# Kernel optimization log

Hardware: AMD Instinct MI355X
Metric: run time of the kernel (lower is better)

## Reference

```python
import jax, jax.numpy as jnp
import numpy as np

B, N, DIN, DOUT, H, E = 8, 512, 128, 128, 8, 16
DH = DOUT // H
SCALE = float(np.sqrt(DH))


def _ln(x, g, b, eps=1e-5):
    m = jnp.mean(x, axis=-1, keepdims=True)
    v = jnp.mean((x - m) ** 2, axis=-1, keepdims=True)
    return (x - m) * jax.lax.rsqrt(v + eps) * g + b


def setup_inputs() -> dict:
    key = jax.random.key(0)
    ks = jax.random.split(key, 12)
    rn = lambda k, s: jax.random.normal(k, s, jnp.float32) * 0.05
    return {
        "x": jax.random.normal(ks[0], (B, N, DIN), jnp.float32),
        "adj": jax.random.randint(ks[1], (B, N, N), 0, 2, jnp.int32),
        "edge_attr": jax.random.normal(ks[2], (B, N, N, E), jnp.float32),
        "ln1_g": jnp.ones((DIN,), jnp.float32), "ln1_b": jnp.zeros((DIN,), jnp.float32),
        "Wp": rn(ks[3], (DIN, DOUT)), "bp": jnp.zeros((DOUT,), jnp.float32),
        "eln_g": jnp.ones((E,), jnp.float32), "eln_b": jnp.zeros((E,), jnp.float32),
        "We1": rn(ks[4], (E, 2 * E)), "be1": jnp.zeros((2 * E,), jnp.float32),
        "We2": rn(ks[5], (2 * E, H)), "be2": jnp.zeros((H,), jnp.float32),
        "Wq": rn(ks[6], (DOUT, DOUT)), "Wk": rn(ks[7], (DOUT, DOUT)), "Wv": rn(ks[8], (DOUT, DOUT)),
        "ffW1": rn(ks[9], (DOUT, 2 * DOUT)), "ffb1": jnp.zeros((2 * DOUT,), jnp.float32),
        "ffW2": rn(ks[10], (2 * DOUT, DOUT)), "ffb2": jnp.zeros((DOUT,), jnp.float32),
        "ln2_g": jnp.ones((DOUT,), jnp.float32), "ln2_b": jnp.zeros((DOUT,), jnp.float32),
    }


def reference(x, adj, edge_attr, ln1_g, ln1_b, Wp, bp, eln_g, eln_b, We1, be1, We2, be2,
              Wq, Wk, Wv, ffW1, ffb1, ffW2, ffb2, ln2_g, ln2_b):
    # Node projection after layer norm: [B,N,DOUT]
    xp = _ln(x, ln1_g, ln1_b) @ Wp + bp

    def heads(W):  # [B,H,N,DH]
        return (xp @ W).reshape(B, N, H, DH).transpose(0, 2, 1, 3)

    Q, K, V = heads(Wq), heads(Wk), heads(Wv)
    s = jnp.einsum('bhnd,bhmd->bhnm', Q, K) / SCALE  # [B,H,N,N]

    # Edge bias MLP: [B,N,N,E] -> [B,N,N,H] -> [B,H,N,N]
    eb = jax.nn.relu(_ln(edge_attr, eln_g, eln_b) @ We1 + be1) @ We2 + be2
    s = s + jnp.tanh(eb).transpose(0, 3, 1, 2) * 5.0

    # LeakyReLU(0.2)
    s = jnp.where(s >= 0, s, 0.2 * s)

    # adjacency mask with self-loops
    eye = jnp.eye(N, dtype=jnp.float32)[None]
    mask = jnp.minimum(adj.astype(jnp.float32) + eye, 1.0)[:, None]  # [B,1,N,N]
    neg_inf = jnp.finfo(s.dtype).min
    s = jnp.where(mask == 0, neg_inf, s)
    all_masked = jnp.all(mask == 0, axis=-1, keepdims=True)
    s = jnp.where(all_masked, 0.0, s)
    s = s - jnp.max(s, axis=-1, keepdims=True)
    p = jnp.nan_to_num(jax.nn.softmax(s, axis=-1))

    ctx = jnp.einsum('bhnm,bhmd->bhnd', p, V).transpose(0, 2, 1, 3).reshape(B, N, DOUT)
    h = xp + ctx
    ffn = jax.nn.relu(_ln(h, ln2_g, ln2_b) @ ffW1 + ffb1) @ ffW2 + ffb2
    return h + ffn
```

## Files before the change

kernel.cpp:

```cpp
#include <hip/hip_runtime.h>
#include <hip/hip_bf16.h>

#define BB 8
#define NN 512
#define DINC 128
#define DOUTC 128
#define HHC 8
#define EEC 16
#define DHC 16

typedef _Float16 h4 __attribute__((ext_vector_type(4)));
typedef float f32x4 __attribute__((ext_vector_type(4)));

__device__ __forceinline__ float wsum(float v){
#pragma unroll
  for (int o=1;o<64;o<<=1) v += __shfl_xor(v,o);
  return v;
}

__global__ __launch_bounds__(256) void k_proj(
    const float* __restrict__ x,
    const float* __restrict__ g1, const float* __restrict__ b1,
    const float* __restrict__ Wp, const float* __restrict__ bp,
    const float* __restrict__ Wq, const float* __restrict__ Wk, const float* __restrict__ Wv,
    float* __restrict__ xp, _Float16* __restrict__ Qh, _Float16* __restrict__ Kh, _Float16* __restrict__ Vh)
{
  __shared__ _Float16 xln[16][136];
  __shared__ _Float16 xps[16][136];
  __shared__ float    xp32[16][132];
  __shared__ _Float16 qs[3][16][136];
  int tid=threadIdx.x, w=tid>>6, lane=tid&63;
  int c=lane&15, g=lane>>4;
  int row0 = blockIdx.x*16;
  int b = row0>>9, n0 = row0&(NN-1);

  float ga=g1[lane], gb=g1[lane+64], ba=b1[lane], bbx=b1[lane+64];
#pragma unroll
  for (int rr=0;rr<4;++rr){
    int r = w + rr*4;
    size_t gi = (size_t)(row0+r)*DINC + lane;
    float a = x[gi], cc = x[gi+64];
    float s = wsum(a+cc);
    float q = wsum(a*a+cc*cc);
    float mean = s*(1.f/DINC);
    float var  = q*(1.f/DINC)-mean*mean;
    float rstd = rsqrtf(var+1e-5f);
    xln[r][lane]    = (_Float16)((a -mean)*rstd*ga + ba);
    xln[r][lane+64] = (_Float16)((cc-mean)*rstd*gb + bbx);
  }
  __syncthreads();

#pragma unroll
  for (int oo=0;oo<2;++oo){
    int ot = 2*w+oo;
    float4 bi = *(const float4*)(bp + 16*ot + 4*g);
    f32x4 D; D[0]=bi.x; D[1]=bi.y; D[2]=bi.z; D[3]=bi.w;
#pragma unroll
    for (int kt=0;kt<8;++kt){
      h4 f;
#pragma unroll
      for (int j=0;j<4;++j)
        f[j] = (_Float16)Wp[(size_t)(16*kt+4*g+j)*DOUTC + 16*ot + c];
      h4 hb = *(const h4*)&xln[c][16*kt+4*g];
      D = __builtin_amdgcn_mfma_f32_16x16x16f16(f, hb, D, 0,0,0);
    }
#pragma unroll
    for (int r=0;r<4;++r){
      xp32[c][16*ot+4*g+r] = D[r];
      xps [c][16*ot+4*g+r] = (_Float16)D[r];
    }
  }
  __syncthreads();

#pragma unroll
  for (int pp=0;pp<6;++pp){
    int p = w + pp*4;
    int mat = p>>3, ot = p&7;
    const float* W = (mat==0)? Wq : ((mat==1)? Wk : Wv);
    f32x4 D = {0.f,0.f,0.f,0.f};
#pragma unroll
    for (int kt=0;kt<8;++kt){
      h4 f;
#pragma unroll
      for (int j=0;j<4;++j)
        f[j] = (_Float16)W[(size_t)(16*kt+4*g+j)*DOUTC + 16*ot + c];
      h4 hb = *(const h4*)&xps[c][16*kt+4*g];
      D = __builtin_amdgcn_mfma_f32_16x16x16f16(f, hb, D, 0,0,0);
    }
#pragma unroll
    for (int r=0;r<4;++r)
      qs[mat][c][16*ot+4*g+r] = (_Float16)D[r];
  }
  __syncthreads();

#pragma unroll
  for (int i=tid;i<512;i+=256){
    int r=i>>5, seg=i&31;
    *(float4*)(xp + (size_t)(row0+r)*DOUTC + seg*4) = *(const float4*)&xp32[r][seg*4];
  }
#pragma unroll
  for (int mat=0;mat<3;++mat){
    int r = tid>>4, seg = tid&15;
    int h = seg>>1, d = (seg&1)*8;
    _Float16* O = (mat==0)? Qh : ((mat==1)? Kh : Vh);
    *(float4*)(O + (((size_t)b*HHC+h)*NN + n0+r)*DHC + d) = *(const float4*)&qs[mat][r][seg*8];
  }
}

__global__ __launch_bounds__(256) void k_edge(
  const float* __restrict__ ea, const int* __restrict__ adj,
  const float* __restrict__ eg, const float* __restrict__ ebi,
  const float* __restrict__ We1, const float* __restrict__ be1,
  const float* __restrict__ We2, const float* __restrict__ be2,
  _Float16* __restrict__ ebias)
{
  __shared__ _Float16 stage[8][520];
  __shared__ unsigned long long msk[8];
  __shared__ unsigned short idx16[512];
  __shared__ int cntS;

  int tid = threadIdx.x, w = tid>>6, lane = tid&63;
  int c = lane&15, g = lane>>4;
  int bn = blockIdx.x;
  int b = bn >> 9, n = bn & (NN-1);

  const int* adjRow = adj + (size_t)bn*NN;
  int col1 = tid, col2 = tid + 256;
  int v1 = (adjRow[col1] != 0) || (col1 == n);
  int v2 = (adjRow[col2] != 0) || (col2 == n);
  unsigned long long b1m = __ballot(v1);
  unsigned long long b2m = __ballot(v2);
  if (lane==0){ msk[w] = b1m; msk[4+w] = b2m; }

  h4 w1a,w1b,w2a,w2b;
#pragma unroll
  for (int j=0;j<4;++j){
    w1a[j] = (_Float16)We1[(4*g+j)*32 + c];
    w1b[j] = (_Float16)We1[(4*g+j)*32 + 16 + c];
    w2a[j] = (_Float16)((c<8)? We2[(4*g+j)*HHC + c] : 0.f);
    w2b[j] = (_Float16)((c<8)? We2[(16+4*g+j)*HHC + c] : 0.f);
  }
  float4 b1a = *(const float4*)(be1 + 4*g);
  float4 b1b = *(const float4*)(be1 + 16 + 4*g);
  float4 b2r = *(const float4*)(be2 + (g&1)*4);
  float4 G4  = *(const float4*)(eg  + 4*g);
  float4 Bv4 = *(const float4*)(ebi + 4*g);

  __syncthreads();

  int offs[8]; int cnt = 0;
#pragma unroll
  for (int k=0;k<8;++k){ offs[k] = cnt; cnt += __popcll(msk[k]); }
  if (tid==0) cntS = cnt;

  {
    _Float16 neg = (_Float16)(-30000.f);
    h4 negv; negv[0]=neg; negv[1]=neg; negv[2]=neg; negv[3]=neg;
#pragma unroll
    for (int i=tid;i<1024;i+=256){
      int h = i>>7, m4 = i&127;
      *(h4*)&stage[h][m4*4] = negv;
    }
  }

  if (v1){
    int pos = offs[w]   + __popcll(msk[w]   & ((1ull<<lane)-1ull));
    idx16[pos] = (unsigned short)col1;
  }
  if (v2){
    int pos = offs[4+w] + __popcll(msk[4+w] & ((1ull<<lane)-1ull));
    idx16[pos] = (unsigned short)col2;
  }
  __syncthreads();

  cnt = cntS;
  int nt = (cnt + 15) >> 4;
  const float* eaRow = ea + (size_t)bn*NN*EEC;

  for (int t = w; t < nt; t += 4){
    int slot = 16*t + c;
    int sidx = slot < cnt ? slot : cnt-1;
    int idx  = idx16[sidx];
    float4 v = *(const float4*)(eaRow + (size_t)idx*EEC + 4*g);
    float s = v.x+v.y+v.z+v.w;
    float q = v.x*v.x+v.y*v.y+v.z*v.z+v.w*v.w;
    s += __shfl_xor(s,16); s += __shfl_xor(s,32);
    q += __shfl_xor(q,16); q += __shfl_xor(q,32);
    float mean = s*(1.f/EEC);
    float var  = q*(1.f/EEC) - mean*mean;
    float rstd = rsqrtf(var + 1e-5f);
    h4 ef;
    ef[0]=(_Float16)((v.x-mean)*rstd*G4.x + Bv4.x);
    ef[1]=(_Float16)((v.y-mean)*rstd*G4.y + Bv4.y);
    ef[2]=(_Float16)((v.z-mean)*rstd*G4.z + Bv4.z);
    ef[3]=(_Float16)((v.w-mean)*rstd*G4.w + Bv4.w);
    f32x4 d1a = {b1a.x,b1a.y,b1a.z,b1a.w};
    f32x4 d1b = {b1b.x,b1b.y,b1b.z,b1b.w};
    d1a = __builtin_amdgcn_mfma_f32_16x16x16f16(w1a, ef, d1a, 0,0,0);
    d1b = __builtin_amdgcn_mfma_f32_16x16x16f16(w1b, ef, d1b, 0,0,0);
    h4 hfa,hfb;
#pragma unroll
    for (int r=0;r<4;++r){
      hfa[r]=(_Float16)fmaxf(d1a[r],0.f);
      hfb[r]=(_Float16)fmaxf(d1b[r],0.f);
    }
    f32x4 d2 = {0.f,0.f,0.f,0.f};
    d2 = __builtin_amdgcn_mfma_f32_16x16x16f16(w2a, hfa, d2, 0,0,0);
    d2 = __builtin_amdgcn_mfma_f32_16x16x16f16(w2b, hfb, d2, 0,0,0);
    if (g<2 && slot<cnt){
#pragma unroll
      for (int r=0;r<4;++r){
        float y = d2[r] + ((const float*)&b2r)[r];
        y = fminf(fmaxf(2.f*y,-30.f),30.f);
        float ex = __expf(y);
        float t2 = (ex-1.f)/(ex+1.f);
        stage[4*g+r][idx] = (_Float16)(5.f*t2);
      }
    }
  }
  __syncthreads();

  size_t base = ((size_t)b*HHC)*NN*NN + (size_t)n*NN;
#pragma unroll
  for (int i=tid;i<512;i+=256){
    int h = i>>6, m8 = i&63;
    *(float4*)(ebias + base + (size_t)h*NN*NN + m8*8) =
        *(const float4*)&stage[h][m8*8];
  }
}

__global__ __launch_bounds__(256) void k_attn(
  const _Float16* __restrict__ Qh, const _Float16* __restrict__ Kh, const _Float16* __restrict__ Vh,
  const _Float16* __restrict__ eb, float* __restrict__ ctxb)
{
  __shared__ _Float16 Klds[NN*DHC];
  __shared__ _Float16 Vt[DHC*520];
  int tid = threadIdx.x;
  int bh   = blockIdx.x >> 3;
  int tile = blockIdx.x & 7;
  const _Float16* Kg = Kh + (size_t)bh*NN*DHC;
  const _Float16* Vg = Vh + (size_t)bh*NN*DHC;
  {
    const float4* src = (const float4*)Kg;
    float4* dst = (float4*)Klds;
#pragma unroll
    for (int i=tid;i<1024;i+=256) dst[i]=src[i];
  }
  {
#pragma unroll
    for (int i=tid;i<1024;i+=256){
      int m = i>>1, hf = i&1;
      float4 v4 = *(const float4*)(Vg + (size_t)m*DHC + hf*8);
      const _Float16* hh = (const _Float16*)&v4;
#pragma unroll
      for (int jj=0;jj<8;++jj) Vt[(hf*8+jj)*520 + m] = hh[jj];
    }
  }
  __syncthreads();

  int w = tid>>6, lane = tid&63;
  int c = lane&15, g = lane>>4;
  int n0 = tile*64 + w*16;

  h4 qf = *(const h4*)(Qh + ((size_t)bh*NN + n0 + c)*DHC + 4*g);
  const _Float16* ebw = eb + ((size_t)bh*NN + n0 + c)*NN + 4*g;

  f32x4 zero = {0.f,0.f,0.f,0.f};
  f32x4 acc = zero;
  float rowsum = 0.f;
#pragma unroll
  for (int t=0;t<32;++t){
    h4 kf = *(const h4*)(Klds + (16*t + c)*DHC + 4*g);
    f32x4 d = __builtin_amdgcn_mfma_f32_16x16x16f16(kf, qf, zero, 0, 0, 0);
    h4 e4 = *(const h4*)(ebw + 16*t);
    h4 pa;
#pragma unroll
    for (int r=0;r<4;++r){
      float sv = d[r]*0.25f + (float)e4[r];
      sv = fmaxf(sv,0.f) + 0.2f*fminf(sv,0.f);
      float p = __expf(sv - 6.f);
      rowsum += p;
      pa[r] = (_Float16)p;
    }
    h4 vf = *(const h4*)(Vt + c*520 + 16*t + 4*g);
    acc = __builtin_amdgcn_mfma_f32_16x16x16f16(pa, vf, acc, 0, 0, 0);
  }
  rowsum += __shfl_xor(rowsum,16);
  rowsum += __shfl_xor(rowsum,32);

  int b = bh>>3, h = bh&7;
#pragma unroll
  for (int r=0;r<4;++r){
    float sr = __shfl(rowsum, g*16 + 4*g + r);
    ctxb[((size_t)b*NN + n0 + 4*g + r)*DOUTC + h*DHC + c] = acc[r]/sr;
  }
}

__global__ __launch_bounds__(256) void k_ffn(
  const float* __restrict__ xp, const float* __restrict__ ctxb,
  const float* __restrict__ g2, const float* __restrict__ b2v,
  const float* __restrict__ W1, const float* __restrict__ bb1,
  const float* __restrict__ W2, const float* __restrict__ bb2,
  float* __restrict__ out)
{
  __shared__ float    hrow[8][DOUTC];
  __shared__ _Float16 hn[16][136];
  __shared__ float    part[4][8][16][16];

  int tid = threadIdx.x, w = tid>>6, lane = tid&63;
  int c = lane&15, g = lane>>4;
  int n0 = blockIdx.x * 8;

#pragma unroll
  for (int i=tid;i<272;i+=256){
    h4 z = {(_Float16)0.f,(_Float16)0.f,(_Float16)0.f,(_Float16)0.f};
    ((h4*)hn)[272+i] = z;
  }

  float ga=g2[lane], gb=g2[lane+64], ba=b2v[lane], bbx=b2v[lane+64];
#pragma unroll
  for (int rr=0;rr<2;++rr){
    int r = w + rr*4;
    size_t gi = (size_t)(n0+r)*DOUTC + lane;
    float a  = xp[gi]    + ctxb[gi];
    float cc = xp[gi+64] + ctxb[gi+64];
    hrow[r][lane] = a; hrow[r][lane+64] = cc;
    float s = wsum(a+cc);
    float q = wsum(a*a+cc*cc);
    float mean = s*(1.f/DOUTC);
    float var  = q*(1.f/DOUTC) - mean*mean;
    float rstd = rsqrtf(var + 1e-5f);
    hn[r][lane]    = (_Float16)((a -mean)*rstd*ga + ba);
    hn[r][lane+64] = (_Float16)((cc-mean)*rstd*gb + bbx);
  }
  __syncthreads();

  h4 hidB[4];
#pragma unroll
  for (int t=0;t<4;++t){
    int ht = 4*w + t;
    float4 bi = *(const float4*)(bb1 + 16*ht + 4*g);
    f32x4 D1; D1[0]=bi.x; D1[1]=bi.y; D1[2]=bi.z; D1[3]=bi.w;
#pragma unroll
    for (int kt=0;kt<8;++kt){
      h4 f;
#pragma unroll
      for (int j=0;j<4;++j)
        f[j] = (_Float16)W1[(size_t)(16*kt + 4*g + j)*256 + 16*ht + c];
      h4 hb = *(const h4*)&hn[c][16*kt + 4*g];
      D1 = __builtin_amdgcn_mfma_f32_16x16x16f16(f, hb, D1, 0,0,0);
    }
#pragma unroll
    for (int r=0;r<4;++r) hidB[t][r] = (_Float16)fmaxf(D1[r], 0.f);
  }

#pragma unroll
  for (int ot=0;ot<8;++ot){
    f32x4 d2 = {0.f,0.f,0.f,0.f};
#pragma unroll
    for (int t=0;t<4;++t){
      h4 f;
#pragma unroll
      for (int j=0;j<4;++j)
        f[j] = (_Float16)W2[(size_t)(16*(4*w+t) + 4*g + j)*128 + 16*ot + c];
      d2 = __builtin_amdgcn_mfma_f32_16x16x16f16(f, hidB[t], d2, 0,0,0);
    }
#pragma unroll
    for (int r=0;r<4;++r) part[w][ot][4*g+r][c] = d2[r];
  }
  __syncthreads();

#pragma unroll
  for (int i=tid;i<1024;i+=256){
    int n = i>>7, col = i&127;
    int ot = col>>4, m = col&15;
    float v = part[0][ot][m][n] + part[1][ot][m][n]
            + part[2][ot][m][n] + part[3][ot][m][n];
    out[(size_t)(n0+n)*DOUTC + col] = hrow[n][col] + v + bb2[col];
  }
}

extern "C" void kernel_launch(void* const* d_in, const int* in_sizes, int n_in,
                              void* d_out, int out_size, void* d_ws, size_t ws_size,
                              hipStream_t stream)
{
  const float* x     = (const float*)d_in[0];
  const int*   adj   = (const int*)  d_in[1];
  const float* ea    = (const float*)d_in[2];
  const float* ln1_g = (const float*)d_in[3];
  const float* ln1_b = (const float*)d_in[4];
  const float* Wp    = (const float*)d_in[5];
  const float* bp    = (const float*)d_in[6];
  const float* eln_g = (const float*)d_in[7];
  const float* eln_b = (const float*)d_in[8];
  const float* We1   = (const float*)d_in[9];
  const float* be1   = (const float*)d_in[10];
  const float* We2   = (const float*)d_in[11];
  const float* be2   = (const float*)d_in[12];
  const float* Wq    = (const float*)d_in[13];
  const float* Wk    = (const float*)d_in[14];
  const float* Wv    = (const float*)d_in[15];
  const float* ffW1  = (const float*)d_in[16];
  const float* ffb1  = (const float*)d_in[17];
  const float* ffW2  = (const float*)d_in[18];
  const float* ffb2  = (const float*)d_in[19];
  const float* ln2_g = (const float*)d_in[20];
  const float* ln2_b = (const float*)d_in[21];
  float* out = (float*)d_out;

  char* ws = (char*)d_ws;
  float*    xp  = (float*)(ws);
  float*    ctx = (float*)(ws + ((size_t)2<<20));
  _Float16* Qh  = (_Float16*)(ws + ((size_t)4<<20));
  _Float16* Kh  = (_Float16*)(ws + ((size_t)5<<20));
  _Float16* Vh  = (_Float16*)(ws + ((size_t)6<<20));
  _Float16* ebf = (_Float16*)(ws + ((size_t)7<<20));

  k_proj<<<(BB*NN)/16, 256, 0, stream>>>(x, ln1_g, ln1_b, Wp, bp, Wq, Wk, Wv, xp, Qh, Kh, Vh);
  k_edge<<<BB*NN, 256, 0, stream>>>(ea, adj, eln_g, eln_b, We1, be1, We2, be2, ebf);
  k_attn<<<BB*HHC*8, 256, 0, stream>>>(Qh, Kh, Vh, ebf, ctx);
  k_ffn<<<(BB*NN)/8, 256, 0, stream>>>(xp, ctx, ln2_g, ln2_b, ffW1, ffb1, ffW2, ffb2, out);
}
```

Before: 79.88 us.

## Merge projection and edge kernels into one launch, restructure edge LN per lane

Combines k_proj and k_edge into a single kernel whose blocks dispatch on blockIdx to either projection or edge work, sharing one shared-memory buffer. This removes one launch and lets the two independent stages run concurrently. The edge path now gives each lane a whole 16-wide edge row for layer norm and stages the results through LDS for four MFMA tiles per wave. xp is stored in fp16 instead of fp32 to cut write and read traffic, at some cost in accuracy for the residual.

```diff
diff --git a/kernel.cpp b/kernel.cpp
--- a/kernel.cpp
+++ b/kernel.cpp
@@ -8,6 +8,7 @@
 #define HHC 8
 #define EEC 16
 #define DHC 16
+#define NPROJ 256
 
 typedef _Float16 h4 __attribute__((ext_vector_type(4)));
 typedef float f32x4 __attribute__((ext_vector_type(4)));
@@ -18,20 +19,21 @@
   return v;
 }
 
-__global__ __launch_bounds__(256) void k_proj(
+
+__device__ __forceinline__ void proj_body(
+    char* smem, int blk,
     const float* __restrict__ x,
     const float* __restrict__ g1, const float* __restrict__ b1,
     const float* __restrict__ Wp, const float* __restrict__ bp,
     const float* __restrict__ Wq, const float* __restrict__ Wk, const float* __restrict__ Wv,
-    float* __restrict__ xp, _Float16* __restrict__ Qh, _Float16* __restrict__ Kh, _Float16* __restrict__ Vh)
-{
-  __shared__ _Float16 xln[16][136];
-  __shared__ _Float16 xps[16][136];
-  __shared__ float    xp32[16][132];
-  __shared__ _Float16 qs[3][16][136];
+    _Float16* __restrict__ xph, _Float16* __restrict__ Qh, _Float16* __restrict__ Kh, _Float16* __restrict__ Vh)
+{
+  _Float16 (*xln)[136] = (_Float16(*)[136])(smem);
+  _Float16 (*xps)[136] = (_Float16(*)[136])(smem + 4352);
+  _Float16* qs         = (_Float16*)(smem + 8704);
   int tid=threadIdx.x, w=tid>>6, lane=tid&63;
   int c=lane&15, g=lane>>4;
-  int row0 = blockIdx.x*16;
+  int row0 = blk*16;
   int b = row0>>9, n0 = row0&(NN-1);
 
   float ga=g1[lane], gb=g1[lane+64], ba=b1[lane], bbx=b1[lane+64];
@@ -65,10 +67,8 @@
       D = __builtin_amdgcn_mfma_f32_16x16x16f16(f, hb, D, 0,0,0);
     }
 #pragma unroll
-    for (int r=0;r<4;++r){
-      xp32[c][16*ot+4*g+r] = D[r];
-      xps [c][16*ot+4*g+r] = (_Float16)D[r];
-    }
+    for (int r=0;r<4;++r)
+      xps[c][16*ot+4*g+r] = (_Float16)D[r];
   }
   __syncthreads();
 
@@ -89,39 +89,39 @@
     }
 #pragma unroll
     for (int r=0;r<4;++r)
-      qs[mat][c][16*ot+4*g+r] = (_Float16)D[r];
-  }
-  __syncthreads();
-
-#pragma unroll
-  for (int i=tid;i<512;i+=256){
-    int r=i>>5, seg=i&31;
-    *(float4*)(xp + (size_t)(row0+r)*DOUTC + seg*4) = *(const float4*)&xp32[r][seg*4];
+      qs[(mat*16 + c)*136 + 16*ot+4*g+r] = (_Float16)D[r];
+  }
+  __syncthreads();
+
+  {
+    int r = tid>>4, seg = tid&15;
+    *(float4*)(xph + (size_t)(row0+r)*DOUTC + seg*8) = *(const float4*)&xps[r][seg*8];
   }
 #pragma unroll
   for (int mat=0;mat<3;++mat){
     int r = tid>>4, seg = tid&15;
     int h = seg>>1, d = (seg&1)*8;
     _Float16* O = (mat==0)? Qh : ((mat==1)? Kh : Vh);
-    *(float4*)(O + (((size_t)b*HHC+h)*NN + n0+r)*DHC + d) = *(const float4*)&qs[mat][r][seg*8];
-  }
-}
-
-__global__ __launch_bounds__(256) void k_edge(
-  const float* __restrict__ ea, const int* __restrict__ adj,
-  const float* __restrict__ eg, const float* __restrict__ ebi,
-  const float* __restrict__ We1, const float* __restrict__ be1,
-  const float* __restrict__ We2, const float* __restrict__ be2,
-  _Float16* __restrict__ ebias)
-{
-  __shared__ _Float16 stage[8][520];
-  __shared__ unsigned long long msk[8];
-  __shared__ unsigned short idx16[512];
-  __shared__ int cntS;
+    *(float4*)(O + (((size_t)b*HHC+h)*NN + n0+r)*DHC + d) = *(const float4*)&qs[(mat*16+r)*136 + seg*8];
+  }
+}
+
+__device__ __forceinline__ void edge_body(
+    char* smem, int bn,
+    const float* __restrict__ ea, const int* __restrict__ adj,
+    const float* __restrict__ eg, const float* __restrict__ ebi,
+    const float* __restrict__ We1, const float* __restrict__ be1,
+    const float* __restrict__ We2, const float* __restrict__ be2,
+    _Float16* __restrict__ ebias)
+{
+  _Float16* ef              = (_Float16*)(smem);
+  _Float16 (*stage)[520]    = (_Float16(*)[520])(smem + 12288);
+  unsigned short* idx16     = (unsigned short*)(smem + 20608);
+  unsigned long long* msk   = (unsigned long long*)(smem + 21632);
+  int* cntS                 = (int*)(smem + 21696);
 
   int tid = threadIdx.x, w = tid>>6, lane = tid&63;
   int c = lane&15, g = lane>>4;
-  int bn = blockIdx.x;
   int b = bn >> 9, n = bn & (NN-1);
 
   const int* adjRow = adj + (size_t)bn*NN;
@@ -140,18 +140,16 @@
     w2a[j] = (_Float16)((c<8)? We2[(4*g+j)*HHC + c] : 0.f);
     w2b[j] = (_Float16)((c<8)? We2[(16+4*g+j)*HHC + c] : 0.f);
   }
+  float4 b2r = *(const float4*)(be2 + (g&1)*4);
   float4 b1a = *(const float4*)(be1 + 4*g);
   float4 b1b = *(const float4*)(be1 + 16 + 4*g);
-  float4 b2r = *(const float4*)(be2 + (g&1)*4);
-  float4 G4  = *(const float4*)(eg  + 4*g);
-  float4 Bv4 = *(const float4*)(ebi + 4*g);
 
   __syncthreads();
 
   int offs[8]; int cnt = 0;
 #pragma unroll
   for (int k=0;k<8;++k){ offs[k] = cnt; cnt += __popcll(msk[k]); }
-  if (tid==0) cntS = cnt;
+  if (tid==0) *cntS = cnt;
 
   {
     _Float16 neg = (_Float16)(-30000.f);
@@ -173,48 +171,59 @@
   }
   __syncthreads();
 
-  cnt = cntS;
-  int nt = (cnt + 15) >> 4;
+  cnt = *cntS;
+  int ng = (cnt + 63) >> 6;
   const float* eaRow = ea + (size_t)bn*NN*EEC;
 
-  for (int t = w; t < nt; t += 4){
-    int slot = 16*t + c;
+  for (int grp = w; grp < ng; grp += 4){
+    int slot = grp*64 + lane;
     int sidx = slot < cnt ? slot : cnt-1;
     int idx  = idx16[sidx];
-    float4 v = *(const float4*)(eaRow + (size_t)idx*EEC + 4*g);
-    float s = v.x+v.y+v.z+v.w;
-    float q = v.x*v.x+v.y*v.y+v.z*v.z+v.w*v.w;
-    s += __shfl_xor(s,16); s += __shfl_xor(s,32);
-    q += __shfl_xor(q,16); q += __shfl_xor(q,32);
+    const float4* ep = (const float4*)(eaRow + (size_t)idx*EEC);
+    float4 a0=ep[0], a1=ep[1], a2=ep[2], a3=ep[3];
+    float e[16] = {a0.x,a0.y,a0.z,a0.w, a1.x,a1.y,a1.z,a1.w,
+                   a2.x,a2.y,a2.z,a2.w, a3.x,a3.y,a3.z,a3.w};
+    float s=0.f, q=0.f;
+#pragma unroll
+    for (int k=0;k<16;++k){ s+=e[k]; q+=e[k]*e[k]; }
     float mean = s*(1.f/EEC);
     float var  = q*(1.f/EEC) - mean*mean;
     float rstd = rsqrtf(var + 1e-5f);
-    h4 ef;
-    ef[0]=(_Float16)((v.x-mean)*rstd*G4.x + Bv4.x);
-    ef[1]=(_Float16)((v.y-mean)*rstd*G4.y + Bv4.y);
-    ef[2]=(_Float16)((v.z-mean)*rstd*G4.z + Bv4.z);
-    ef[3]=(_Float16)((v.w-mean)*rstd*G4.w + Bv4.w);
-    f32x4 d1a = {b1a.x,b1a.y,b1a.z,b1a.w};
-    f32x4 d1b = {b1b.x,b1b.y,b1b.z,b1b.w};
-    d1a = __builtin_amdgcn_mfma_f32_16x16x16f16(w1a, ef, d1a, 0,0,0);
-    d1b = __builtin_amdgcn_mfma_f32_16x16x16f16(w1b, ef, d1b, 0,0,0);
-    h4 hfa,hfb;
-#pragma unroll
-    for (int r=0;r<4;++r){
-      hfa[r]=(_Float16)fmaxf(d1a[r],0.f);
-      hfb[r]=(_Float16)fmaxf(d1b[r],0.f);
-    }
-    f32x4 d2 = {0.f,0.f,0.f,0.f};
-    d2 = __builtin_amdgcn_mfma_f32_16x16x16f16(w2a, hfa, d2, 0,0,0);
-    d2 = __builtin_amdgcn_mfma_f32_16x16x16f16(w2b, hfb, d2, 0,0,0);
-    if (g<2 && slot<cnt){
+    _Float16 ef16[16];
+#pragma unroll
+    for (int k=0;k<16;++k)
+      ef16[k] = (_Float16)((e[k]-mean)*rstd*eg[k] + ebi[k]);
+    _Float16* dst = ef + (size_t)(w*64 + lane)*24;
+    *(float4*)(dst)     = *(const float4*)&ef16[0];
+    *(float4*)(dst + 8) = *(const float4*)&ef16[8];
+
+#pragma unroll
+    for (int tt=0;tt<4;++tt){
+      h4 efr = *(const h4*)(ef + (size_t)(w*64 + tt*16 + c)*24 + 4*g);
+      f32x4 d1a = {b1a.x,b1a.y,b1a.z,b1a.w};
+      f32x4 d1b = {b1b.x,b1b.y,b1b.z,b1b.w};
+      d1a = __builtin_amdgcn_mfma_f32_16x16x16f16(w1a, efr, d1a, 0,0,0);
+      d1b = __builtin_amdgcn_mfma_f32_16x16x16f16(w1b, efr, d1b, 0,0,0);
+      h4 hfa,hfb;
 #pragma unroll
       for (int r=0;r<4;++r){
-        float y = d2[r] + ((const float*)&b2r)[r];
-        y = fminf(fmaxf(2.f*y,-30.f),30.f);
-        float ex = __expf(y);
-        float t2 = (ex-1.f)/(ex+1.f);
-        stage[4*g+r][idx] = (_Float16)(5.f*t2);
+        hfa[r]=(_Float16)fmaxf(d1a[r],0.f);
+        hfb[r]=(_Float16)fmaxf(d1b[r],0.f);
+      }
+      f32x4 d2 = {0.f,0.f,0.f,0.f};
+      d2 = __builtin_amdgcn_mfma_f32_16x16x16f16(w2a, hfa, d2, 0,0,0);
+      d2 = __builtin_amdgcn_mfma_f32_16x16x16f16(w2b, hfb, d2, 0,0,0);
+      int slot2 = grp*64 + tt*16 + c;
+      if (g<2 && slot2<cnt){
+        int sidx2 = idx16[slot2];
+#pragma unroll
+        for (int r=0;r<4;++r){
+          float y = d2[r] + ((const float*)&b2r)[r];
+          y = fminf(fmaxf(2.f*y,-30.f),30.f);
+          float ex = __expf(y);
+          float t2 = (ex-1.f)/(ex+1.f);
+          stage[4*g+r][sidx2] = (_Float16)(5.f*t2);
+        }
       }
     }
   }
@@ -227,6 +236,26 @@
     *(float4*)(ebias + base + (size_t)h*NN*NN + m8*8) =
         *(const float4*)&stage[h][m8*8];
   }
+}
+
+__global__ __launch_bounds__(256) void k_projedge(
+    const float* __restrict__ x,
+    const float* __restrict__ g1, const float* __restrict__ b1,
+    const float* __restrict__ Wp, const float* __restrict__ bp,
+    const float* __restrict__ Wq, const float* __restrict__ Wk, const float* __restrict__ Wv,
+    _Float16* __restrict__ xph, _Float16* __restrict__ Qh, _Float16* __restrict__ Kh, _Float16* __restrict__ Vh,
+    const float* __restrict__ ea, const int* __restrict__ adj,
+    const float* __restrict__ eg, const float* __restrict__ ebi,
+    const float* __restrict__ We1, const float* __restrict__ be1,
+    const float* __restrict__ We2, const float* __restrict__ be2,
+    _Float16* __restrict__ ebias)
+{
+  __shared__ __align__(16) char smem[21760];
+  int blk = blockIdx.x;
+  if (blk < NPROJ)
+    proj_body(smem, blk, x, g1, b1, Wp, bp, Wq, Wk, Wv, xph, Qh, Kh, Vh);
+  else
+    edge_body(smem, blk - NPROJ, ea, adj, eg, ebi, We1, be1, We2, be2, ebias);
 }
 
 __global__ __launch_bounds__(256) void k_attn(
@@ -297,7 +326,7 @@
 }
 
 __global__ __launch_bounds__(256) void k_ffn(
-  const float* __restrict__ xp, const float* __restrict__ ctxb,
+  const _Float16* __restrict__ xph, const float* __restrict__ ctxb,
   const float* __restrict__ g2, const float* __restrict__ b2v,
   const float* __restrict__ W1, const float* __restrict__ bb1,
   const float* __restrict__ W2, const float* __restrict__ bb2,
@@ -322,8 +351,8 @@
   for (int rr=0;rr<2;++rr){
     int r = w + rr*4;
     size_t gi = (size_t)(n0+r)*DOUTC + lane;
-    float a  = xp[gi]    + ctxb[gi];
-    float cc = xp[gi+64] + ctxb[gi+64];
+    float a  = (float)xph[gi]    + ctxb[gi];
+    float cc = (float)xph[gi+64] + ctxb[gi+64];
     hrow[r][lane] = a; hrow[r][lane+64] = cc;
     float s = wsum(a+cc);
     float q = wsum(a*a+cc*cc);
@@ -409,15 +438,16 @@
   float* out = (float*)d_out;
 
   char* ws = (char*)d_ws;
-  float*    xp  = (float*)(ws);
+  _Float16* xph = (_Float16*)(ws);
   float*    ctx = (float*)(ws + ((size_t)2<<20));
   _Float16* Qh  = (_Float16*)(ws + ((size_t)4<<20));
   _Float16* Kh  = (_Float16*)(ws + ((size_t)5<<20));
   _Float16* Vh  = (_Float16*)(ws + ((size_t)6<<20));
   _Float16* ebf = (_Float16*)(ws + ((size_t)7<<20));
 
-  k_proj<<<(BB*NN)/16, 256, 0, stream>>>(x, ln1_g, ln1_b, Wp, bp, Wq, Wk, Wv, xp, Qh, Kh, Vh);
-  k_edge<<<BB*NN, 256, 0, stream>>>(ea, adj, eln_g, eln_b, We1, be1, We2, be2, ebf);
+  k_projedge<<<NPROJ + BB*NN, 256, 0, stream>>>(
+      x, ln1_g, ln1_b, Wp, bp, Wq, Wk, Wv, xph, Qh, Kh, Vh,
+      ea, adj, eln_g, eln_b, We1, be1, We2, be2, ebf);
   k_attn<<<BB*HHC*8, 256, 0, stream>>>(Qh, Kh, Vh, ebf, ctx);
-  k_ffn<<<(BB*NN)/8, 256, 0, stream>>>(xp, ctx, ln2_g, ln2_b, ffW1, ffb1, ffW2, ffb2, out);
-}
+  k_ffn<<<(BB*NN)/8, 256, 0, stream>>>(xph, ctx, ln2_g, ln2_b, ffW1, ffb1, ffW2, ffb2, out);
+}
```

After: 89.23 us. +11.7%, slower.

## Merge projection and edge-bias kernels into one launch; store xp in fp16

Applied to the files above, without the earlier changes.

Combines the node projection kernel and the edge-bias MLP kernel into a single grid. Edge blocks come first and projection blocks are appended, which removes one launch and lets the two independent stages overlap on the GPU. The residual xp is also stored as fp16 instead of fp32, so k_ffn reads half as many bytes for it. The cost is lower precision in the residual path, and every block now reserves the combined shared memory of both stages, which may reduce occupancy.

```diff
diff --git a/kernel.cpp b/kernel.cpp
--- a/kernel.cpp
+++ b/kernel.cpp
@@ -8,6 +8,7 @@
 #define HHC 8
 #define EEC 16
 #define DHC 16
+#define NEDGE (BB*NN)
 
 typedef _Float16 h4 __attribute__((ext_vector_type(4)));
 typedef float f32x4 __attribute__((ext_vector_type(4)));
@@ -18,214 +19,209 @@
   return v;
 }
 
-__global__ __launch_bounds__(256) void k_proj(
+__global__ __launch_bounds__(256) void k_projedge(
     const float* __restrict__ x,
     const float* __restrict__ g1, const float* __restrict__ b1,
     const float* __restrict__ Wp, const float* __restrict__ bp,
     const float* __restrict__ Wq, const float* __restrict__ Wk, const float* __restrict__ Wv,
-    float* __restrict__ xp, _Float16* __restrict__ Qh, _Float16* __restrict__ Kh, _Float16* __restrict__ Vh)
-{
-  __shared__ _Float16 xln[16][136];
-  __shared__ _Float16 xps[16][136];
-  __shared__ float    xp32[16][132];
-  __shared__ _Float16 qs[3][16][136];
-  int tid=threadIdx.x, w=tid>>6, lane=tid&63;
-  int c=lane&15, g=lane>>4;
-  int row0 = blockIdx.x*16;
-  int b = row0>>9, n0 = row0&(NN-1);
-
-  float ga=g1[lane], gb=g1[lane+64], ba=b1[lane], bbx=b1[lane+64];
-#pragma unroll
-  for (int rr=0;rr<4;++rr){
-    int r = w + rr*4;
-    size_t gi = (size_t)(row0+r)*DINC + lane;
-    float a = x[gi], cc = x[gi+64];
-    float s = wsum(a+cc);
-    float q = wsum(a*a+cc*cc);
-    float mean = s*(1.f/DINC);
-    float var  = q*(1.f/DINC)-mean*mean;
-    float rstd = rsqrtf(var+1e-5f);
-    xln[r][lane]    = (_Float16)((a -mean)*rstd*ga + ba);
-    xln[r][lane+64] = (_Float16)((cc-mean)*rstd*gb + bbx);
-  }
-  __syncthreads();
-
-#pragma unroll
-  for (int oo=0;oo<2;++oo){
-    int ot = 2*w+oo;
-    float4 bi = *(const float4*)(bp + 16*ot + 4*g);
-    f32x4 D; D[0]=bi.x; D[1]=bi.y; D[2]=bi.z; D[3]=bi.w;
-#pragma unroll
-    for (int kt=0;kt<8;++kt){
-      h4 f;
-#pragma unroll
-      for (int j=0;j<4;++j)
-        f[j] = (_Float16)Wp[(size_t)(16*kt+4*g+j)*DOUTC + 16*ot + c];
-      h4 hb = *(const h4*)&xln[c][16*kt+4*g];
-      D = __builtin_amdgcn_mfma_f32_16x16x16f16(f, hb, D, 0,0,0);
-    }
-#pragma unroll
-    for (int r=0;r<4;++r){
-      xp32[c][16*ot+4*g+r] = D[r];
-      xps [c][16*ot+4*g+r] = (_Float16)D[r];
-    }
-  }
-  __syncthreads();
-
-#pragma unroll
-  for (int pp=0;pp<6;++pp){
-    int p = w + pp*4;
-    int mat = p>>3, ot = p&7;
-    const float* W = (mat==0)? Wq : ((mat==1)? Wk : Wv);
-    f32x4 D = {0.f,0.f,0.f,0.f};
-#pragma unroll
-    for (int kt=0;kt<8;++kt){
-      h4 f;
-#pragma unroll
-      for (int j=0;j<4;++j)
-        f[j] = (_Float16)W[(size_t)(16*kt+4*g+j)*DOUTC + 16*ot + c];
-      h4 hb = *(const h4*)&xps[c][16*kt+4*g];
-      D = __builtin_amdgcn_mfma_f32_16x16x16f16(f, hb, D, 0,0,0);
-    }
-#pragma unroll
-    for (int r=0;r<4;++r)
-      qs[mat][c][16*ot+4*g+r] = (_Float16)D[r];
-  }
-  __syncthreads();
-
-#pragma unroll
-  for (int i=tid;i<512;i+=256){
-    int r=i>>5, seg=i&31;
-    *(float4*)(xp + (size_t)(row0+r)*DOUTC + seg*4) = *(const float4*)&xp32[r][seg*4];
-  }
-#pragma unroll
-  for (int mat=0;mat<3;++mat){
-    int r = tid>>4, seg = tid&15;
-    int h = seg>>1, d = (seg&1)*8;
-    _Float16* O = (mat==0)? Qh : ((mat==1)? Kh : Vh);
-    *(float4*)(O + (((size_t)b*HHC+h)*NN + n0+r)*DHC + d) = *(const float4*)&qs[mat][r][seg*8];
-  }
-}
-
-__global__ __launch_bounds__(256) void k_edge(
-  const float* __restrict__ ea, const int* __restrict__ adj,
-  const float* __restrict__ eg, const float* __restrict__ ebi,
-  const float* __restrict__ We1, const float* __restrict__ be1,
-  const float* __restrict__ We2, const float* __restrict__ be2,
-  _Float16* __restrict__ ebias)
+    _Float16* __restrict__ xph, _Float16* __restrict__ Qh, _Float16* __restrict__ Kh, _Float16* __restrict__ Vh,
+    const float* __restrict__ ea, const int* __restrict__ adj,
+    const float* __restrict__ eg, const float* __restrict__ ebi,
+    const float* __restrict__ We1, const float* __restrict__ be1,
+    const float* __restrict__ We2, const float* __restrict__ be2,
+    _Float16* __restrict__ ebias)
 {
   __shared__ _Float16 stage[8][520];
   __shared__ unsigned long long msk[8];
   __shared__ unsigned short idx16[512];
   __shared__ int cntS;
+  __shared__ _Float16 xln[16][136];
+  __shared__ _Float16 xps[16][136];
+  __shared__ _Float16 qs[3][16][136];
 
   int tid = threadIdx.x, w = tid>>6, lane = tid&63;
   int c = lane&15, g = lane>>4;
-  int bn = blockIdx.x;
-  int b = bn >> 9, n = bn & (NN-1);
-
-  const int* adjRow = adj + (size_t)bn*NN;
-  int col1 = tid, col2 = tid + 256;
-  int v1 = (adjRow[col1] != 0) || (col1 == n);
-  int v2 = (adjRow[col2] != 0) || (col2 == n);
-  unsigned long long b1m = __ballot(v1);
-  unsigned long long b2m = __ballot(v2);
-  if (lane==0){ msk[w] = b1m; msk[4+w] = b2m; }
-
-  h4 w1a,w1b,w2a,w2b;
-#pragma unroll
-  for (int j=0;j<4;++j){
-    w1a[j] = (_Float16)We1[(4*g+j)*32 + c];
-    w1b[j] = (_Float16)We1[(4*g+j)*32 + 16 + c];
-    w2a[j] = (_Float16)((c<8)? We2[(4*g+j)*HHC + c] : 0.f);
-    w2b[j] = (_Float16)((c<8)? We2[(16+4*g+j)*HHC + c] : 0.f);
-  }
-  float4 b1a = *(const float4*)(be1 + 4*g);
-  float4 b1b = *(const float4*)(be1 + 16 + 4*g);
-  float4 b2r = *(const float4*)(be2 + (g&1)*4);
-  float4 G4  = *(const float4*)(eg  + 4*g);
-  float4 Bv4 = *(const float4*)(ebi + 4*g);
-
-  __syncthreads();
-
-  int offs[8]; int cnt = 0;
-#pragma unroll
-  for (int k=0;k<8;++k){ offs[k] = cnt; cnt += __popcll(msk[k]); }
-  if (tid==0) cntS = cnt;
-
-  {
-    _Float16 neg = (_Float16)(-30000.f);
-    h4 negv; negv[0]=neg; negv[1]=neg; negv[2]=neg; negv[3]=neg;
-#pragma unroll
-    for (int i=tid;i<1024;i+=256){
-      int h = i>>7, m4 = i&127;
-      *(h4*)&stage[h][m4*4] = negv;
-    }
-  }
-
-  if (v1){
-    int pos = offs[w]   + __popcll(msk[w]   & ((1ull<<lane)-1ull));
-    idx16[pos] = (unsigned short)col1;
-  }
-  if (v2){
-    int pos = offs[4+w] + __popcll(msk[4+w] & ((1ull<<lane)-1ull));
-    idx16[pos] = (unsigned short)col2;
-  }
-  __syncthreads();
-
-  cnt = cntS;
-  int nt = (cnt + 15) >> 4;
-  const float* eaRow = ea + (size_t)bn*NN*EEC;
-
-  for (int t = w; t < nt; t += 4){
-    int slot = 16*t + c;
-    int sidx = slot < cnt ? slot : cnt-1;
-    int idx  = idx16[sidx];
-    float4 v = *(const float4*)(eaRow + (size_t)idx*EEC + 4*g);
-    float s = v.x+v.y+v.z+v.w;
-    float q = v.x*v.x+v.y*v.y+v.z*v.z+v.w*v.w;
-    s += __shfl_xor(s,16); s += __shfl_xor(s,32);
-    q += __shfl_xor(q,16); q += __shfl_xor(q,32);
-    float mean = s*(1.f/EEC);
-    float var  = q*(1.f/EEC) - mean*mean;
-    float rstd = rsqrtf(var + 1e-5f);
-    h4 ef;
-    ef[0]=(_Float16)((v.x-mean)*rstd*G4.x + Bv4.x);
-    ef[1]=(_Float16)((v.y-mean)*rstd*G4.y + Bv4.y);
-    ef[2]=(_Float16)((v.z-mean)*rstd*G4.z + Bv4.z);
-    ef[3]=(_Float16)((v.w-mean)*rstd*G4.w + Bv4.w);
-    f32x4 d1a = {b1a.x,b1a.y,b1a.z,b1a.w};
-    f32x4 d1b = {b1b.x,b1b.y,b1b.z,b1b.w};
-    d1a = __builtin_amdgcn_mfma_f32_16x16x16f16(w1a, ef, d1a, 0,0,0);
-    d1b = __builtin_amdgcn_mfma_f32_16x16x16f16(w1b, ef, d1b, 0,0,0);
-    h4 hfa,hfb;
-#pragma unroll
-    for (int r=0;r<4;++r){
-      hfa[r]=(_Float16)fmaxf(d1a[r],0.f);
-      hfb[r]=(_Float16)fmaxf(d1b[r],0.f);
-    }
-    f32x4 d2 = {0.f,0.f,0.f,0.f};
-    d2 = __builtin_amdgcn_mfma_f32_16x16x16f16(w2a, hfa, d2, 0,0,0);
-    d2 = __builtin_amdgcn_mfma_f32_16x16x16f16(w2b, hfb, d2, 0,0,0);
-    if (g<2 && slot<cnt){
+
+  if (blockIdx.x < NEDGE){
+    int bn = blockIdx.x;
+    int b = bn >> 9, n = bn & (NN-1);
+
+    const int* adjRow = adj + (size_t)bn*NN;
+    int col1 = tid, col2 = tid + 256;
+    int v1 = (adjRow[col1] != 0) || (col1 == n);
+    int v2 = (adjRow[col2] != 0) || (col2 == n);
+    unsigned long long b1m = __ballot(v1);
+    unsigned long long b2m = __ballot(v2);
+    if (lane==0){ msk[w] = b1m; msk[4+w] = b2m; }
+
+    h4 w1a,w1b,w2a,w2b;
+#pragma unroll
+    for (int j=0;j<4;++j){
+      w1a[j] = (_Float16)We1[(4*g+j)*32 + c];
+      w1b[j] = (_Float16)We1[(4*g+j)*32 + 16 + c];
+      w2a[j] = (_Float16)((c<8)? We2[(4*g+j)*HHC + c] : 0.f);
+      w2b[j] = (_Float16)((c<8)? We2[(16+4*g+j)*HHC + c] : 0.f);
+    }
+    float4 b1a = *(const float4*)(be1 + 4*g);
+    float4 b1b = *(const float4*)(be1 + 16 + 4*g);
+    float4 b2r = *(const float4*)(be2 + (g&1)*4);
+    float4 G4  = *(const float4*)(eg  + 4*g);
+    float4 Bv4 = *(const float4*)(ebi + 4*g);
+
+    __syncthreads();
+
+    int offs[8]; int cnt = 0;
+#pragma unroll
+    for (int k=0;k<8;++k){ offs[k] = cnt; cnt += __popcll(msk[k]); }
+    if (tid==0) cntS = cnt;
+
+    {
+      _Float16 neg = (_Float16)(-30000.f);
+      h4 negv; negv[0]=neg; negv[1]=neg; negv[2]=neg; negv[3]=neg;
+#pragma unroll
+      for (int i=tid;i<1024;i+=256){
+        int h = i>>7, m4 = i&127;
+        *(h4*)&stage[h][m4*4] = negv;
+      }
+    }
+
+    if (v1){
+      int pos = offs[w]   + __popcll(msk[w]   & ((1ull<<lane)-1ull));
+      idx16[pos] = (unsigned short)col1;
+    }
+    if (v2){
+      int pos = offs[4+w] + __popcll(msk[4+w] & ((1ull<<lane)-1ull));
+      idx16[pos] = (unsigned short)col2;
+    }
+    __syncthreads();
+
+    cnt = cntS;
+    int nt = (cnt + 15) >> 4;
+    const float* eaRow = ea + (size_t)bn*NN*EEC;
+
+    for (int t = w; t < nt; t += 4){
+      int slot = 16*t + c;
+      int sidx = slot < cnt ? slot : cnt-1;
+      int idx  = idx16[sidx];
+      float4 v = *(const float4*)(eaRow + (size_t)idx*EEC + 4*g);
+      float s = v.x+v.y+v.z+v.w;
+      float q = v.x*v.x+v.y*v.y+v.z*v.z+v.w*v.w;
+      s += __shfl_xor(s,16); s += __shfl_xor(s,32);
+      q += __shfl_xor(q,16); q += __shfl_xor(q,32);
+      float mean = s*(1.f/EEC);
+      float var  = q*(1.f/EEC) - mean*mean;
+      float rstd = rsqrtf(var + 1e-5f);
+      h4 ef;
+      ef[0]=(_Float16)((v.x-mean)*rstd*G4.x + Bv4.x);
+      ef[1]=(_Float16)((v.y-mean)*rstd*G4.y + Bv4.y);
+      ef[2]=(_Float16)((v.z-mean)*rstd*G4.z + Bv4.z);
+      ef[3]=(_Float16)((v.w-mean)*rstd*G4.w + Bv4.w);
+      f32x4 d1a = {b1a.x,b1a.y,b1a.z,b1a.w};
+      f32x4 d1b = {b1b.x,b1b.y,b1b.z,b1b.w};
+      d1a = __builtin_amdgcn_mfma_f32_16x16x16f16(w1a, ef, d1a, 0,0,0);
+      d1b = __builtin_amdgcn_mfma_f32_16x16x16f16(w1b, ef, d1b, 0,0,0);
+      h4 hfa,hfb;
 #pragma unroll
       for (int r=0;r<4;++r){
-        float y = d2[r] + ((const float*)&b2r)[r];
-        y = fminf(fmaxf(2.f*y,-30.f),30.f);
-        float ex = __expf(y);
-        float t2 = (ex-1.f)/(ex+1.f);
-        stage[4*g+r][idx] = (_Float16)(5.f*t2);
+        hfa[r]=(_Float16)fmaxf(d1a[r],0.f);
+        hfb[r]=(_Float16)fmaxf(d1b[r],0.f);
       }
-    }
-  }
-  __syncthreads();
-
-  size_t base = ((size_t)b*HHC)*NN*NN + (size_t)n*NN;
-#pragma unroll
-  for (int i=tid;i<512;i+=256){
-    int h = i>>6, m8 = i&63;
-    *(float4*)(ebias + base + (size_t)h*NN*NN + m8*8) =
-        *(const float4*)&stage[h][m8*8];
+      f32x4 d2 = {0.f,0.f,0.f,0.f};
+      d2 = __builtin_amdgcn_mfma_f32_16x16x16f16(w2a, hfa, d2, 0,0,0);
+      d2 = __builtin_amdgcn_mfma_f32_16x16x16f16(w2b, hfb, d2, 0,0,0);
+      if (g<2 && slot<cnt){
+#pragma unroll
+        for (int r=0;r<4;++r){
+          float y = d2[r] + ((const float*)&b2r)[r];
+          y = fminf(fmaxf(2.f*y,-30.f),30.f);
+          float ex = __expf(y);
+          float t2 = (ex-1.f)/(ex+1.f);
+          stage[4*g+r][idx] = (_Float16)(5.f*t2);
+        }
+      }
+    }
+    __syncthreads();
+
+    size_t base = ((size_t)b*HHC)*NN*NN + (size_t)n*NN;
+#pragma unroll
+    for (int i=tid;i<512;i+=256){
+      int h = i>>6, m8 = i&63;
+      *(float4*)(ebias + base + (size_t)h*NN*NN + m8*8) =
+          *(const float4*)&stage[h][m8*8];
+    }
+  } else {
+    int blk = blockIdx.x - NEDGE;
+    int row0 = blk*16;
+    int b = row0>>9, n0 = row0&(NN-1);
+
+    float ga=g1[lane], gb=g1[lane+64], ba=b1[lane], bbx=b1[lane+64];
+#pragma unroll
+    for (int rr=0;rr<4;++rr){
+      int r = w + rr*4;
+      size_t gi = (size_t)(row0+r)*DINC + lane;
+      float a = x[gi], cc = x[gi+64];
+      float s = wsum(a+cc);
+      float q = wsum(a*a+cc*cc);
+      float mean = s*(1.f/DINC);
+      float var  = q*(1.f/DINC)-mean*mean;
+      float rstd = rsqrtf(var+1e-5f);
+      xln[r][lane]    = (_Float16)((a -mean)*rstd*ga + ba);
+      xln[r][lane+64] = (_Float16)((cc-mean)*rstd*gb + bbx);
+    }
+    __syncthreads();
+
+#pragma unroll
+    for (int oo=0;oo<2;++oo){
+      int ot = 2*w+oo;
+      float4 bi = *(const float4*)(bp + 16*ot + 4*g);
+      f32x4 D; D[0]=bi.x; D[1]=bi.y; D[2]=bi.z; D[3]=bi.w;
+#pragma unroll
+      for (int kt=0;kt<8;++kt){
+        h4 f;
+#pragma unroll
+        for (int j=0;j<4;++j)
+          f[j] = (_Float16)Wp[(size_t)(16*kt+4*g+j)*DOUTC + 16*ot + c];
+        h4 hb = *(const h4*)&xln[c][16*kt+4*g];
+        D = __builtin_amdgcn_mfma_f32_16x16x16f16(f, hb, D, 0,0,0);
+      }
+#pragma unroll
+      for (int r=0;r<4;++r)
+        xps[c][16*ot+4*g+r] = (_Float16)D[r];
+    }
+    __syncthreads();
+
+#pragma unroll
+    for (int pp=0;pp<6;++pp){
+      int p = w + pp*4;
+      int mat = p>>3, ot = p&7;
+      const float* W = (mat==0)? Wq : ((mat==1)? Wk : Wv);
+      f32x4 D = {0.f,0.f,0.f,0.f};
+#pragma unroll
+      for (int kt=0;kt<8;++kt){
+        h4 f;
+#pragma unroll
+        for (int j=0;j<4;++j)
+          f[j] = (_Float16)W[(size_t)(16*kt+4*g+j)*DOUTC + 16*ot + c];
+        h4 hb = *(const h4*)&xps[c][16*kt+4*g];
+        D = __builtin_amdgcn_mfma_f32_16x16x16f16(f, hb, D, 0,0,0);
+      }
+#pragma unroll
+      for (int r=0;r<4;++r)
+        qs[mat][c][16*ot+4*g+r] = (_Float16)D[r];
+    }
+    __syncthreads();
+
+    {
+      int r = tid>>4, seg = tid&15;
+      *(float4*)(xph + (size_t)(row0+r)*DOUTC + seg*8) = *(const float4*)&xps[r][seg*8];
+    }
+#pragma unroll
+    for (int mat=0;mat<3;++mat){
+      int r = tid>>4, seg = tid&15;
+      int h = seg>>1, d = (seg&1)*8;
+      _Float16* O = (mat==0)? Qh : ((mat==1)? Kh : Vh);
+      *(float4*)(O + (((size_t)b*HHC+h)*NN + n0+r)*DHC + d) = *(const float4*)&qs[mat][r][seg*8];
+    }
   }
 }
 
@@ -297,7 +293,7 @@
 }
 
 __global__ __launch_bounds__(256) void k_ffn(
-  const float* __restrict__ xp, const float* __restrict__ ctxb,
+  const _Float16* __restrict__ xph, const float* __restrict__ ctxb,
   const float* __restrict__ g2, const float* __restrict__ b2v,
   const float* __restrict__ W1, const float* __restrict__ bb1,
   const float* __restrict__ W2, const float* __restrict__ bb2,
@@ -322,8 +318,8 @@
   for (int rr=0;rr<2;++rr){
     int r = w + rr*4;
     size_t gi = (size_t)(n0+r)*DOUTC + lane;
-    float a  = xp[gi]    + ctxb[gi];
-    float cc = xp[gi+64] + ctxb[gi+64];
+    float a  = (float)xph[gi]    + ctxb[gi];
+    float cc = (float)xph[gi+64] + ctxb[gi+64];
     hrow[r][lane] = a; hrow[r][lane+64] = cc;
     float s = wsum(a+cc);
     float q = wsum(a*a+cc*cc);
@@ -409,15 +405,16 @@
   float* out = (float*)d_out;
 
   char* ws = (char*)d_ws;
-  float*    xp  = (float*)(ws);
+  _Float16* xph = (_Float16*)(ws);
   float*    ctx = (float*)(ws + ((size_t)2<<20));
   _Float16* Qh  = (_Float16*)(ws + ((size_t)4<<20));
   _Float16* Kh  = (_Float16*)(ws + ((size_t)5<<20));
   _Float16* Vh  = (_Float16*)(ws + ((size_t)6<<20));
   _Float16* ebf = (_Float16*)(ws + ((size_t)7<<20));
 
-  k_proj<<<(BB*NN)/16, 256, 0, stream>>>(x, ln1_g, ln1_b, Wp, bp, Wq, Wk, Wv, xp, Qh, Kh, Vh);
-  k_edge<<<BB*NN, 256, 0, stream>>>(ea, adj, eln_g, eln_b, We1, be1, We2, be2, ebf);
+  k_projedge<<<NEDGE + (BB*NN)/16, 256, 0, stream>>>(
+      x, ln1_g, ln1_b, Wp, bp, Wq, Wk, Wv, xph, Qh, Kh, Vh,
+      ea, adj, eln_g, eln_b, We1, be1, We2, be2, ebf);
   k_attn<<<BB*HHC*8, 256, 0, stream>>>(Qh, Kh, Vh, ebf, ctx);
-  k_ffn<<<(BB*NN)/8, 256, 0, stream>>>(xp, ctx, ln2_g, ln2_b, ffW1, ffb1, ffW2, ffb2, out);
+  k_ffn<<<(BB*NN)/8, 256, 0, stream>>>(xph, ctx, ln2_g, ln2_b, ffW1, ffb1, ffW2, ffb2, out);
 }
```

New measurement: 84.87 us. +6.2%, slower.
